# Kernel optimization log

Measured on AMD Instinct MI355X. Metric: run time of the kernel, lower is better.

## Reference

```python
import jax, jax.numpy as jnp
import numpy as np
from jax import lax

B, T = 16, 1000
IN_DIM = 257
CTX = 3            # left + 1 + right
FEAT = CTX * IN_DIM  # 771
H = 512
L = 2              # SRU layers
KN = 9             # conv kernels
KS = 6             # conv kernel size


def setup_inputs() -> dict:
    key = jax.random.key(0)
    ks = jax.random.split(key, 10)
    n = jax.random.normal
    return {
        "inputs": n(ks[0], (B, T, FEAT), jnp.float32),
        "W_in": n(ks[1], (FEAT, H), jnp.float32) / np.sqrt(FEAT),
        "b_in": jnp.zeros((H,), jnp.float32),
        "W_rnn": n(ks[2], (L, H, 3 * H), jnp.float32) / np.sqrt(H),
        "v_rnn": n(ks[3], (L, 2 * H), jnp.float32) * 0.1,
        "b_rnn": jnp.zeros((L, 2 * H), jnp.float32),
        "conv_k": n(ks[4], (KN, 1, KS, KS), jnp.float32) * 0.05,
        "conv_b": jnp.zeros((KN,), jnp.float32),
        "W_out": n(ks[5], (H * KN, FEAT), jnp.float32) / np.sqrt(H * KN),
        "b_out": jnp.zeros((FEAT,), jnp.float32),
    }


def _sru_layer(x, W, v, b):
    # x: (T, B, H) time-major; SRU: c_t = f_t*c_{t-1} + (1-f_t)*(W x_t),
    # highway h_t = r_t*c_t + (1-r_t)*x_t; gates peek at c_{t-1} via v.
    U = jnp.einsum("tbh,hk->tbk", x, W)          # (T, B, 3H)
    xt, fp, rp = jnp.split(U, 3, axis=-1)
    vf, vr = jnp.split(v, 2)
    bf, br = jnp.split(b, 2)

    def step(c, inp):
        xt_t, fp_t, rp_t, xin_t = inp
        f = jax.nn.sigmoid(fp_t + vf * c + bf)
        c_new = f * c + (1.0 - f) * xt_t
        r = jax.nn.sigmoid(rp_t + vr * c + br)
        h = r * c_new + (1.0 - r) * xin_t
        return c_new, h

    c0 = jnp.zeros(x.shape[1:], x.dtype)
    _, hs = lax.scan(step, c0, (xt, fp, rp, x))
    return hs


def reference(inputs, W_in, b_in, W_rnn, v_rnn, b_rnn, conv_k, conv_b, W_out, b_out):
    # input layer: Linear + Tanh
    h = jnp.tanh(jnp.einsum("btf,fh->bth", inputs, W_in) + b_in)  # (B,T,H)
    x = jnp.transpose(h, (1, 0, 2))                               # (T,B,H)
    for l in range(L):
        x = _sru_layer(x, W_rnn[l], v_rnn[l], b_rnn[l])
    h = jnp.transpose(x, (1, 0, 2))[:, None]                      # (B,1,T,H)

    # Conv2d with asymmetric pad (left/top 3, right/bottom 2), +bias, tanh
    y = lax.conv_general_dilated(
        h, conv_k, window_strides=(1, 1), padding=[(3, 2), (3, 2)],
        dimension_numbers=("NCHW", "OIHW", "NCHW"))
    y = jnp.tanh(y + conv_b[None, :, None, None])                 # (B,KN,T,H)
    # MaxPool2d(3, stride=1, padding=1)
    y = lax.reduce_window(y, -jnp.inf, lax.max, (1, 1, 3, 3), (1, 1, 1, 1),
                          [(0, 0), (0, 0), (1, 1), (1, 1)])

    # (B,KN,T,H) -> (B,T,H,KN) -> (B,T,H*KN)  (matches torch double transpose)
    y = jnp.transpose(y, (0, 2, 3, 1)).reshape(B, T, H * KN)
    mask = jax.nn.sigmoid(jnp.einsum("btf,fo->bto", y, W_out) + b_out)
    out = mask * inputs
    return out[:, :, IN_DIM:2 * IN_DIM]  # center frame (left_context slice)
```

## Files before the change

kernel.cpp:

```cpp
#include <hip/hip_runtime.h>
#include <hip/hip_bf16.h>

#define B_    16
#define T_    1000
#define FEAT  771
#define FEATP 800
#define H_    512
#define H3    1536
#define KN_   9
#define KHID  4608
#define M_    16000
#define NOUT  257
#define KSLICES 3

typedef _Float16 half8 __attribute__((ext_vector_type(8)));
typedef _Float16 half4 __attribute__((ext_vector_type(4)));
typedef _Float16 half2v __attribute__((ext_vector_type(2)));
typedef _Float16 h2 __attribute__((ext_vector_type(2)));
typedef float    floatx4 __attribute__((ext_vector_type(4)));

__device__ inline float tanh_fast(float z) {
    return 1.0f - 2.0f / (1.0f + __expf(2.0f * z));
}
__device__ inline float sigmoid_fast(float z) {
    return 1.0f / (1.0f + __expf(-z));
}

__device__ inline void gload16(const _Float16* g, _Float16* l) {
    __builtin_amdgcn_global_load_lds(
        (const __attribute__((address_space(1))) void*)g,
        (__attribute__((address_space(3))) void*)l, 16, 0, 0);
}

__device__ inline void pk_fma_acc(unsigned& acc, unsigned w, unsigned x) {
    asm("v_pk_fma_f16 %0, %1, %2, %0" : "+v"(acc) : "s"(w), "v"(x));
}
__device__ inline unsigned pk_max(unsigned a, unsigned b) {
    unsigned d;
    asm("v_pk_max_f16 %0, %1, %2" : "=v"(d) : "v"(a), "v"(b));
    return d;
}

__global__ void convert_inputs(const float* __restrict__ in, _Float16* __restrict__ A1) {
    size_t i = (size_t)blockIdx.x * 256 + threadIdx.x;
    if (i >= (size_t)M_ * FEATP) return;
    size_t r = i / FEATP;
    int   cc = (int)(i % FEATP);
    A1[i] = (cc < FEAT) ? (_Float16)in[r * FEAT + cc] : (_Float16)0.f;
}

__global__ void pack_ck(const float* __restrict__ ck, unsigned int* __restrict__ ckp) {
    const int i = threadIdx.x;
    if (i < 9 * 36) {
        const _Float16 w = (_Float16)ck[i];
        const unsigned short u = __builtin_bit_cast(unsigned short, w);
        ckp[i] = ((unsigned int)u << 16) | u;
    }
}

__global__ __launch_bounds__(256) void transpose_w(
    const float* __restrict__ W, _Float16* __restrict__ Wt,
    int K, int N, int ldw, int coloff, int Kp, int perm9)
{
    __shared__ float tile[32][33];
    const int kb = blockIdx.x * 32;
    const int nb = blockIdx.y * 32;
    const int tx = threadIdx.x & 31;
    const int ty = threadIdx.x >> 5;
    #pragma unroll
    for (int r = ty; r < 32; r += 8) {
        const int k = kb + r, n = nb + tx;
        tile[r][tx] = (k < K && n < N) ? W[(size_t)k * ldw + coloff + n] : 0.f;
    }
    __syncthreads();
    #pragma unroll
    for (int r = ty; r < 32; r += 8) {
        const int n = nb + r, k = kb + tx;
        if (n < N && k < Kp) {
            size_t kidx = (size_t)k;
            if (perm9) kidx = (size_t)(k % 9) * 512 + (size_t)(k / 9);
            Wt[(size_t)n * Kp + kidx] = (_Float16)tile[tx][r];
        }
    }
}

template <int EPI>
__global__ __launch_bounds__(256) void gemm_kernel(
    const _Float16* __restrict__ A, const _Float16* __restrict__ Bt,
    int Kp, int nk, int Nb,
    _Float16* __restrict__ Ch, float* __restrict__ Cf, int ldc,
    const float* __restrict__ bias)
{
    __shared__ __align__(16) _Float16 As[2][128][32];
    __shared__ __align__(16) _Float16 Bs[2][128][32];

    const int tid  = threadIdx.x;
    const int m0   = blockIdx.x * 128;
    const int n0   = blockIdx.y * 128;
    const int koff = blockIdx.z * (nk << 5);
    const int wave = tid >> 6;
    const int lane = tid & 63;
    const int wr   = (wave >> 1) << 6;
    const int wc   = (wave & 1) << 6;
    const int lrow = lane & 15;
    const int lq   = lane >> 4;

    const int srow0  = wave * 32 + (lane >> 2);
    const int schunk = (lane & 3) * 8;
    const _Float16* aSrc = A  + (size_t)(m0 + srow0) * Kp + koff + schunk;
    const _Float16* bSrc = Bt + (size_t)(n0 + srow0) * Kp + koff + schunk;
    const size_t rstep = (size_t)16 * Kp;

    floatx4 acc[4][4];
    #pragma unroll
    for (int i = 0; i < 4; ++i)
        #pragma unroll
        for (int j = 0; j < 4; ++j)
            #pragma unroll
            for (int r = 0; r < 4; ++r) acc[i][j][r] = 0.f;

    gload16(aSrc,         &As[0][wave * 32][0]);
    gload16(aSrc + rstep, &As[0][wave * 32 + 16][0]);
    gload16(bSrc,         &Bs[0][wave * 32][0]);
    gload16(bSrc + rstep, &Bs[0][wave * 32 + 16][0]);
    asm volatile("s_waitcnt vmcnt(0)" ::: "memory");
    __builtin_amdgcn_s_barrier();

    for (int kc = 0; kc < nk; ++kc) {
        const int cur = kc & 1;
        if (kc + 1 < nk) {
            const _Float16* a2 = aSrc + (size_t)(kc + 1) * 32;
            const _Float16* b2 = bSrc + (size_t)(kc + 1) * 32;
            gload16(a2,         &As[cur ^ 1][wave * 32][0]);
            gload16(a2 + rstep, &As[cur ^ 1][wave * 32 + 16][0]);
            gload16(b2,         &Bs[cur ^ 1][wave * 32][0]);
            gload16(b2 + rstep, &Bs[cur ^ 1][wave * 32 + 16][0]);
        }

        half8 af[4], bfr[4];
        #pragma unroll
        for (int i = 0; i < 4; ++i) af[i]  = *(const half8*)(&As[cur][wr + i * 16 + lrow][lq * 8]);
        #pragma unroll
        for (int j = 0; j < 4; ++j) bfr[j] = *(const half8*)(&Bs[cur][wc + j * 16 + lrow][lq * 8]);
        #pragma unroll
        for (int i = 0; i < 4; ++i)
            #pragma unroll
            for (int j = 0; j < 4; ++j)
                acc[i][j] = __builtin_amdgcn_mfma_f32_16x16x32_f16(af[i], bfr[j], acc[i][j], 0, 0, 0);

        if (kc + 1 < nk) {
            asm volatile("s_waitcnt vmcnt(0)" ::: "memory");
            __builtin_amdgcn_s_barrier();
        }
    }

    #pragma unroll
    for (int j = 0; j < 4; ++j) {
        const int col = n0 + wc + j * 16 + lrow;
        if (col >= Nb) continue;
        #pragma unroll
        for (int i = 0; i < 4; ++i) {
            #pragma unroll
            for (int r = 0; r < 4; ++r) {
                const int row = m0 + wr + i * 16 + lq * 4 + r;
                float v = acc[i][j][r];
                if constexpr (EPI == 0) {
                    float z = v + bias[col];
                    Ch[(size_t)row * ldc + col] = (_Float16)tanh_fast(z);
                } else if constexpr (EPI == 1) {
                    Ch[(size_t)(col >> 9) * ((size_t)M_ * 512) + (size_t)row * 512 + (col & 511)] = (_Float16)v;
                } else {
                    Cf[(size_t)blockIdx.z * M_ * NOUT + (size_t)row * NOUT + col] = v;
                }
            }
        }
    }
}

__global__ __launch_bounds__(256) void reduce_out(
    const float* __restrict__ Cp, const float* __restrict__ bias,
    const float* __restrict__ aux, float* __restrict__ out)
{
    const size_t i = (size_t)blockIdx.x * 256 + threadIdx.x;
    if (i >= (size_t)M_ * NOUT) return;
    const int row = (int)(i / NOUT);
    const int col = (int)(i % NOUT);
    float s = Cp[i] + Cp[i + (size_t)M_ * NOUT] + Cp[i + 2 * (size_t)M_ * NOUT];
    out[i] = sigmoid_fast(s + bias[col]) * aux[(size_t)row * FEAT + 257 + col];
}

__global__ __launch_bounds__(64) void sru_scan(
    const _Float16* __restrict__ U,
    const _Float16* __restrict__ X,
    _Float16* __restrict__ Xout,
    const float* __restrict__ v, const float* __restrict__ bg)
{
    __shared__ __align__(16) _Float16 lds[2][4][40][64];
    const int tid = threadIdx.x;
    const int b   = blockIdx.x >> 3;
    const int h0  = (blockIdx.x & 7) << 6;
    const int h   = h0 + tid;
    const float vf = v[h],       vr = v[512 + h];
    const float bf = bg[h],      br = bg[512 + h];

    const _Float16* plane0 = U;
    const _Float16* plane1 = U + (size_t)M_ * 512;
    const _Float16* plane2 = U + 2 * (size_t)M_ * 512;
    const _Float16* plane3 = X;

    const int lrow = tid >> 3;
    const int lcol = (tid & 7) * 8;

    _Float16* ox = Xout + (size_t)b * T_ * 512 + h;

    auto refill = [&](int bufi, int t0) {
        const size_t rbase = (size_t)(b * T_ + t0 + lrow) * 512 + h0 + lcol;
        #pragma unroll
        for (int j = 0; j < 5; ++j) {
            const size_t o = rbase + (size_t)(8 * j) * 512;
            gload16(plane0 + o, &lds[bufi][0][8 * j][0]);
            gload16(plane1 + o, &lds[bufi][1][8 * j][0]);
            gload16(plane2 + o, &lds[bufi][2][8 * j][0]);
            gload16(plane3 + o, &lds[bufi][3][8 * j][0]);
        }
    };

    refill(0, 0);
    float c = 0.f;
    int cur = 0;
    for (int tb = 0; tb < 25; ++tb) {
        const int t0 = tb * 40;
        if (tb + 1 < 25) {
            refill(cur ^ 1, t0 + 40);
            asm volatile("s_waitcnt vmcnt(20)" ::: "memory");
        } else {
            asm volatile("s_waitcnt vmcnt(0)" ::: "memory");
        }
        __builtin_amdgcn_sched_barrier(0);
        #pragma unroll
        for (int j = 0; j < 40; ++j) {
            const float xt = (float)lds[cur][0][j][tid];
            const float fp = (float)lds[cur][1][j][tid];
            const float rp = (float)lds[cur][2][j][tid];
            const float x  = (float)lds[cur][3][j][tid];
            const float f  = sigmoid_fast(fp + vf * c + bf);
            const float r  = sigmoid_fast(rp + vr * c + br);
            const float cn = f * c + (1.0f - f) * xt;
            const float hO = r * cn + (1.0f - r) * x;
            ox[(size_t)(t0 + j) * 512] = (_Float16)hO;
            c = cn;
        }
        cur ^= 1;
    }
}

#define CVW 76

__global__ __launch_bounds__(320) void conv_pool(
    const _Float16* __restrict__ X, const unsigned int* __restrict__ ckp,
    const float* __restrict__ cb, _Float16* __restrict__ A3)
{
    __shared__ __align__(16) _Float16 in_s[23][80];
    __shared__ __align__(16) _Float16 cv[9][18][CVW];
    const int tid = threadIdx.x;
    int bi = blockIdx.x;
    const int th = bi & 7;  bi >>= 3;
    const int tt = bi % 63;
    const int b  = bi / 63;
    const int t0 = tt * 16, h0 = th * 64;

    for (int i = tid; i < 23 * 76; i += 320) {
        const int r = i / 76, cc = i % 76;
        const int gt = t0 - 4 + r, gh = h0 - 4 + cc;
        _Float16 val = (_Float16)0.f;
        if (gt >= 0 && gt < T_ && gh >= 0 && gh < H_)
            val = X[((size_t)b * T_ + gt) * H_ + gh];
        in_s[r][cc] = val;
    }
    __syncthreads();

    if (tid < 306) {
        const int pt = tid / 17;
        const int co = (tid % 17) * 4;

        const int ct = t0 - 1 + pt;
        const bool rok = (ct >= 0) && (ct < T_);
        const int chb = h0 - 1 + co;
        const bool ok0 = rok && (chb + 0 >= 0) && (chb + 0 < H_);
        const bool ok1 = rok && (chb + 1 >= 0) && (chb + 1 < H_);
        const bool ok2 = rok && (chb + 2 >= 0) && (chb + 2 < H_);
        const bool ok3 = rok && (chb + 3 >= 0) && (chb + 3 < H_);

        unsigned acc0[9], acc1[9];
        #pragma unroll
        for (int k = 0; k < 9; ++k) { acc0[k] = 0u; acc1[k] = 0u; }

        #pragma unroll 1
        for (int ii = 0; ii < 6; ++ii) {
            const unsigned int* rw = (const unsigned int*)&in_s[pt + ii][co];
            const uint2 a01 = *(const uint2*)(rw);
            const uint2 a23 = *(const uint2*)(rw + 2);
            const unsigned int A0 = a01.x, A1v = a01.y, A2 = a23.x, A3v = a23.y;
            const unsigned int A4 = rw[4];
            const unsigned int M0 = __builtin_amdgcn_alignbit(A1v, A0, 16);
            const unsigned int M1 = __builtin_amdgcn_alignbit(A2, A1v, 16);
            const unsigned int M2 = __builtin_amdgcn_alignbit(A3v, A2, 16);
            const unsigned int M3 = __builtin_amdgcn_alignbit(A4, A3v, 16);

            const unsigned int* wt = ckp + ii * 6;
            #pragma unroll
            for (int k = 0; k < 9; ++k) {
                const unsigned int* wk = wt + k * 36;
                pk_fma_acc(acc0[k], wk[0], A0);   pk_fma_acc(acc1[k], wk[0], A1v);
                pk_fma_acc(acc0[k], wk[1], M0);   pk_fma_acc(acc1[k], wk[1], M1);
                pk_fma_acc(acc0[k], wk[2], A1v);  pk_fma_acc(acc1[k], wk[2], A2);
                pk_fma_acc(acc0[k], wk[3], M1);   pk_fma_acc(acc1[k], wk[3], M2);
                pk_fma_acc(acc0[k], wk[4], A2);   pk_fma_acc(acc1[k], wk[4], A3v);
                pk_fma_acc(acc0[k], wk[5], M2);   pk_fma_acc(acc1[k], wk[5], M3);
            }
        }

        const _Float16 NEG = (_Float16)(-65504.f);
        #pragma unroll
        for (int k = 0; k < 9; ++k) {
            const h2 pa = __builtin_bit_cast(h2, acc0[k]);
            const h2 pb = __builtin_bit_cast(h2, acc1[k]);
            half4 o;
            o[0] = ok0 ? pa[0] : NEG;
            o[1] = ok1 ? pa[1] : NEG;
            o[2] = ok2 ? pb[0] : NEG;
            o[3] = ok3 ? pb[1] : NEG;
            *(half4*)(&cv[k][pt][co]) = o;
        }
    }
    __syncthreads();

    if (tid < 256) {
        const int pt = tid >> 4;
        const int gt = t0 + pt;
        if (gt < T_) {
            const int ph = (tid & 15) * 4;
            _Float16* dst = A3 + ((size_t)b * T_ + gt) * KHID + (h0 + ph);
            #pragma unroll
            for (int k = 0; k < 9; ++k) {
                unsigned q01 = 0xFC00FC00u, q23 = 0xFC00FC00u;
                #pragma unroll
                for (int dr = 0; dr < 3; ++dr) {
                    const unsigned* cr = (const unsigned*)&cv[k][pt + dr][ph];
                    const uint2 w01 = *(const uint2*)(cr);
                    const unsigned w2 = cr[2];
                    const unsigned m12 = __builtin_amdgcn_alignbit(w01.y, w01.x, 16);
                    const unsigned m34 = __builtin_amdgcn_alignbit(w2, w01.y, 16);
                    q01 = pk_max(q01, pk_max(pk_max(w01.x, m12), w01.y));
                    q23 = pk_max(q23, pk_max(pk_max(w01.y, m34), w2));
                }
                const h2 qa = __builtin_bit_cast(h2, q01);
                const h2 qb = __builtin_bit_cast(h2, q23);
                const float bk = cb[k];
                half4 o;
                o[0] = (_Float16)tanh_fast((float)qa[0] + bk);
                o[1] = (_Float16)tanh_fast((float)qa[1] + bk);
                o[2] = (_Float16)tanh_fast((float)qb[0] + bk);
                o[3] = (_Float16)tanh_fast((float)qb[1] + bk);
                *(half4*)(dst + (size_t)k * 512) = o;
            }
        }
    }
}

extern "C" void kernel_launch(void* const* d_in, const int* in_sizes, int n_in,
                              void* d_out, int out_size, void* d_ws, size_t ws_size,
                              hipStream_t stream) {
    const float* inputs = (const float*)d_in[0];
    const float* W_in   = (const float*)d_in[1];
    const float* b_in   = (const float*)d_in[2];
    const float* W_rnn  = (const float*)d_in[3];
    const float* v_rnn  = (const float*)d_in[4];
    const float* b_rnn  = (const float*)d_in[5];
    const float* conv_k = (const float*)d_in[6];
    const float* conv_b = (const float*)d_in[7];
    const float* W_out  = (const float*)d_in[8];
    const float* b_out  = (const float*)d_in[9];
    float* out = (float*)d_out;

    char* ws = (char*)d_ws;
    size_t off = 0;
    auto take = [&](size_t bytes) -> char* {
        off = (off + 255) & ~(size_t)255;
        char* p = ws + off;
        off += bytes;
        return p;
    };
    _Float16* W3T  = (_Float16*)take((size_t)NOUT * KHID * 2);
    _Float16* A1   = (_Float16*)take((size_t)M_ * FEATP * 2);
    _Float16* W1T  = (_Float16*)take((size_t)H_ * FEATP * 2);
    _Float16* W2T0 = (_Float16*)take((size_t)H3 * H_ * 2);
    _Float16* W2T1 = (_Float16*)take((size_t)H3 * H_ * 2);
    _Float16* X0   = (_Float16*)take((size_t)M_ * H_ * 2);
    _Float16* X1   = (_Float16*)take((size_t)M_ * H_ * 2);
    _Float16* U    = (_Float16*)take(3 * (size_t)M_ * 512 * 2);
    _Float16* A3   = (_Float16*)take((size_t)M_ * KHID * 2);
    unsigned int* ckp = (unsigned int*)take(9 * 36 * 4);
    float* Cp = (float*)A1;
    _Float16* X2 = X0;

    {
        size_t n = (size_t)M_ * FEATP;
        convert_inputs<<<dim3((unsigned)((n + 255) / 256)), 256, 0, stream>>>(inputs, A1);
    }
    pack_ck<<<dim3(1), 384, 0, stream>>>(conv_k, ckp);
    transpose_w<<<dim3(25, 16), 256, 0, stream>>>(W_in, W1T, FEAT, H_, H_, 0, FEATP, 0);
    transpose_w<<<dim3(16, 48), 256, 0, stream>>>(W_rnn, W2T0, H_, H3, H3, 0, H_, 0);
    transpose_w<<<dim3(16, 48), 256, 0, stream>>>(W_rnn + (size_t)H_ * H3, W2T1, H_, H3, H3, 0, H_, 0);
    transpose_w<<<dim3(144, 9), 256, 0, stream>>>(W_out, W3T, KHID, NOUT, FEAT, 257, KHID, 1);

    gemm_kernel<0><<<dim3(125, 4), 256, 0, stream>>>(A1, W1T, FEATP, 25, H_, X0, nullptr, H_, b_in);

    gemm_kernel<1><<<dim3(125, 12), 256, 0, stream>>>(X0, W2T0, H_, 16, H3, U, nullptr, 0, nullptr);
    sru_scan<<<dim3(128), 64, 0, stream>>>(U, X0, X1, v_rnn, b_rnn);

    gemm_kernel<1><<<dim3(125, 12), 256, 0, stream>>>(X1, W2T1, H_, 16, H3, U, nullptr, 0, nullptr);
    sru_scan<<<dim3(128), 64, 0, stream>>>(U, X1, X2, v_rnn + 1024, b_rnn + 1024);

    conv_pool<<<dim3(16 * 63 * 8), 320, 0, stream>>>(X2, ckp, conv_b, A3);

    gemm_kernel<3><<<dim3(125, 3, KSLICES), 256, 0, stream>>>(A3, W3T, KHID, 144 / KSLICES, NOUT, nullptr, Cp, 0, nullptr);
    {
        const unsigned nred = (unsigned)(((size_t)M_ * NOUT + 255) / 256);
        reduce_out<<<dim3(nred), 256, 0, stream>>>(Cp, b_out + 257, inputs, out);
    }
}
```

Baseline: 727.0 us.

## Skip dead MFMA tiles in ragged output GEMM, fuse setup kernels, cut split-K

The final GEMM gains a ragged mode in which waves and 16-column fragments lying entirely past N=257 skip their LDS loads and MFMAs, removing wasted tensor work in the third N-block. Split-K drops from 3 to 2 slices, so the reduce pass reads one fewer partial buffer at the cost of fewer blocks in flight. The conv-kernel packing is folded into the input-convert kernel, and the two RNN weight transposes are merged into one launch, reducing launch count. The maxpool is reordered to take the vertical max first and then the horizontal one, sharing work across the two output pairs.

```diff
diff --git a/kernel.cpp b/kernel.cpp
--- a/kernel.cpp
+++ b/kernel.cpp
@@ -11,7 +11,7 @@
 #define KHID  4608
 #define M_    16000
 #define NOUT  257
-#define KSLICES 3
+#define KSLICES 2
 
 typedef _Float16 half8 __attribute__((ext_vector_type(8)));
 typedef _Float16 half4 __attribute__((ext_vector_type(4)));
@@ -41,7 +41,15 @@
     return d;
 }
 
-__global__ void convert_inputs(const float* __restrict__ in, _Float16* __restrict__ A1) {
+__global__ void convert_inputs(const float* __restrict__ in, _Float16* __restrict__ A1,
+                               const float* __restrict__ ck, unsigned int* __restrict__ ckp) {
+    if (blockIdx.x == 0) {
+        for (int j = threadIdx.x; j < 9 * 36; j += 256) {
+            const _Float16 w = (_Float16)ck[j];
+            const unsigned short u = __builtin_bit_cast(unsigned short, w);
+            ckp[j] = ((unsigned int)u << 16) | u;
+        }
+    }
     size_t i = (size_t)blockIdx.x * 256 + threadIdx.x;
     if (i >= (size_t)M_ * FEATP) return;
     size_t r = i / FEATP;
@@ -49,19 +57,13 @@
     A1[i] = (cc < FEAT) ? (_Float16)in[r * FEAT + cc] : (_Float16)0.f;
 }
 
-__global__ void pack_ck(const float* __restrict__ ck, unsigned int* __restrict__ ckp) {
-    const int i = threadIdx.x;
-    if (i < 9 * 36) {
-        const _Float16 w = (_Float16)ck[i];
-        const unsigned short u = __builtin_bit_cast(unsigned short, w);
-        ckp[i] = ((unsigned int)u << 16) | u;
-    }
-}
-
 __global__ __launch_bounds__(256) void transpose_w(
     const float* __restrict__ W, _Float16* __restrict__ Wt,
-    int K, int N, int ldw, int coloff, int Kp, int perm9)
+    int K, int N, int ldw, int coloff, int Kp, int perm9,
+    size_t zsrc, size_t zdst)
 {
+    W  += (size_t)blockIdx.z * zsrc;
+    Wt += (size_t)blockIdx.z * zdst;
     __shared__ float tile[32][33];
     const int kb = blockIdx.x * 32;
     const int nb = blockIdx.y * 32;
@@ -84,7 +86,7 @@
     }
 }
 
-template <int EPI>
+template <int EPI, int RAG>
 __global__ __launch_bounds__(256) void gemm_kernel(
     const _Float16* __restrict__ A, const _Float16* __restrict__ Bt,
     int Kp, int nk, int Nb,
@@ -104,6 +106,7 @@
     const int wc   = (wave & 1) << 6;
     const int lrow = lane & 15;
     const int lq   = lane >> 4;
+    const bool waveAlive = !RAG || (n0 + wc < Nb);
 
     const int srow0  = wave * 32 + (lane >> 2);
     const int schunk = (lane & 3) * 8;
@@ -137,16 +140,23 @@
             gload16(b2 + rstep, &Bs[cur ^ 1][wave * 32 + 16][0]);
         }
 
-        half8 af[4], bfr[4];
-        #pragma unroll
-        for (int i = 0; i < 4; ++i) af[i]  = *(const half8*)(&As[cur][wr + i * 16 + lrow][lq * 8]);
-        #pragma unroll
-        for (int j = 0; j < 4; ++j) bfr[j] = *(const half8*)(&Bs[cur][wc + j * 16 + lrow][lq * 8]);
-        #pragma unroll
-        for (int i = 0; i < 4; ++i)
-            #pragma unroll
-            for (int j = 0; j < 4; ++j)
-                acc[i][j] = __builtin_amdgcn_mfma_f32_16x16x32_f16(af[i], bfr[j], acc[i][j], 0, 0, 0);
+        if (waveAlive) {
+            half8 af[4], bfr[4];
+            #pragma unroll
+            for (int i = 0; i < 4; ++i) af[i] = *(const half8*)(&As[cur][wr + i * 16 + lrow][lq * 8]);
+            #pragma unroll
+            for (int j = 0; j < 4; ++j) {
+                if (RAG && n0 + wc + j * 16 >= Nb) continue;
+                bfr[j] = *(const half8*)(&Bs[cur][wc + j * 16 + lrow][lq * 8]);
+            }
+            #pragma unroll
+            for (int i = 0; i < 4; ++i)
+                #pragma unroll
+                for (int j = 0; j < 4; ++j) {
+                    if (RAG && n0 + wc + j * 16 >= Nb) continue;
+                    acc[i][j] = __builtin_amdgcn_mfma_f32_16x16x32_f16(af[i], bfr[j], acc[i][j], 0, 0, 0);
+                }
+        }
 
         if (kc + 1 < nk) {
             asm volatile("s_waitcnt vmcnt(0)" ::: "memory");
@@ -185,7 +195,7 @@
     if (i >= (size_t)M_ * NOUT) return;
     const int row = (int)(i / NOUT);
     const int col = (int)(i % NOUT);
-    float s = Cp[i] + Cp[i + (size_t)M_ * NOUT] + Cp[i + 2 * (size_t)M_ * NOUT];
+    float s = Cp[i] + Cp[i + (size_t)M_ * NOUT];
     out[i] = sigmoid_fast(s + bias[col]) * aux[(size_t)row * FEAT + 257 + col];
 }
 
@@ -343,17 +353,19 @@
             _Float16* dst = A3 + ((size_t)b * T_ + gt) * KHID + (h0 + ph);
             #pragma unroll
             for (int k = 0; k < 9; ++k) {
-                unsigned q01 = 0xFC00FC00u, q23 = 0xFC00FC00u;
-                #pragma unroll
-                for (int dr = 0; dr < 3; ++dr) {
-                    const unsigned* cr = (const unsigned*)&cv[k][pt + dr][ph];
-                    const uint2 w01 = *(const uint2*)(cr);
-                    const unsigned w2 = cr[2];
-                    const unsigned m12 = __builtin_amdgcn_alignbit(w01.y, w01.x, 16);
-                    const unsigned m34 = __builtin_amdgcn_alignbit(w2, w01.y, 16);
-                    q01 = pk_max(q01, pk_max(pk_max(w01.x, m12), w01.y));
-                    q23 = pk_max(q23, pk_max(pk_max(w01.y, m34), w2));
-                }
+                const unsigned* c0 = (const unsigned*)&cv[k][pt + 0][ph];
+                const unsigned* c1 = (const unsigned*)&cv[k][pt + 1][ph];
+                const unsigned* c2 = (const unsigned*)&cv[k][pt + 2][ph];
+                const uint2 x0 = *(const uint2*)c0;  const unsigned y0 = c0[2];
+                const uint2 x1 = *(const uint2*)c1;  const unsigned y1 = c1[2];
+                const uint2 x2 = *(const uint2*)c2;  const unsigned y2 = c2[2];
+                const unsigned VA = pk_max(pk_max(x0.x, x1.x), x2.x);
+                const unsigned VB = pk_max(pk_max(x0.y, x1.y), x2.y);
+                const unsigned VC = pk_max(pk_max(y0,   y1),   y2);
+                const unsigned m12 = __builtin_amdgcn_alignbit(VB, VA, 16);
+                const unsigned m34 = __builtin_amdgcn_alignbit(VC, VB, 16);
+                const unsigned q01 = pk_max(pk_max(VA, m12), VB);
+                const unsigned q23 = pk_max(pk_max(VB, m34), VC);
                 const h2 qa = __builtin_bit_cast(h2, q01);
                 const h2 qb = __builtin_bit_cast(h2, q23);
                 const float bk = cb[k];
@@ -406,25 +418,24 @@
 
     {
         size_t n = (size_t)M_ * FEATP;
-        convert_inputs<<<dim3((unsigned)((n + 255) / 256)), 256, 0, stream>>>(inputs, A1);
-    }
-    pack_ck<<<dim3(1), 384, 0, stream>>>(conv_k, ckp);
-    transpose_w<<<dim3(25, 16), 256, 0, stream>>>(W_in, W1T, FEAT, H_, H_, 0, FEATP, 0);
-    transpose_w<<<dim3(16, 48), 256, 0, stream>>>(W_rnn, W2T0, H_, H3, H3, 0, H_, 0);
-    transpose_w<<<dim3(16, 48), 256, 0, stream>>>(W_rnn + (size_t)H_ * H3, W2T1, H_, H3, H3, 0, H_, 0);
-    transpose_w<<<dim3(144, 9), 256, 0, stream>>>(W_out, W3T, KHID, NOUT, FEAT, 257, KHID, 1);
-
-    gemm_kernel<0><<<dim3(125, 4), 256, 0, stream>>>(A1, W1T, FEATP, 25, H_, X0, nullptr, H_, b_in);
-
-    gemm_kernel<1><<<dim3(125, 12), 256, 0, stream>>>(X0, W2T0, H_, 16, H3, U, nullptr, 0, nullptr);
+        convert_inputs<<<dim3((unsigned)((n + 255) / 256)), 256, 0, stream>>>(inputs, A1, conv_k, ckp);
+    }
+    transpose_w<<<dim3(25, 16), 256, 0, stream>>>(W_in, W1T, FEAT, H_, H_, 0, FEATP, 0, 0, 0);
+    transpose_w<<<dim3(16, 48, 2), 256, 0, stream>>>(W_rnn, W2T0, H_, H3, H3, 0, H_, 0,
+                                                     (size_t)H_ * H3, (size_t)H3 * H_);
+    transpose_w<<<dim3(144, 9), 256, 0, stream>>>(W_out, W3T, KHID, NOUT, FEAT, 257, KHID, 1, 0, 0);
+
+    gemm_kernel<0, 0><<<dim3(125, 4), 256, 0, stream>>>(A1, W1T, FEATP, 25, H_, X0, nullptr, H_, b_in);
+
+    gemm_kernel<1, 0><<<dim3(125, 12), 256, 0, stream>>>(X0, W2T0, H_, 16, H3, U, nullptr, 0, nullptr);
     sru_scan<<<dim3(128), 64, 0, stream>>>(U, X0, X1, v_rnn, b_rnn);
 
-    gemm_kernel<1><<<dim3(125, 12), 256, 0, stream>>>(X1, W2T1, H_, 16, H3, U, nullptr, 0, nullptr);
+    gemm_kernel<1, 0><<<dim3(125, 12), 256, 0, stream>>>(X1, W2T1, H_, 16, H3, U, nullptr, 0, nullptr);
     sru_scan<<<dim3(128), 64, 0, stream>>>(U, X1, X2, v_rnn + 1024, b_rnn + 1024);
 
     conv_pool<<<dim3(16 * 63 * 8), 320, 0, stream>>>(X2, ckp, conv_b, A3);
 
-    gemm_kernel<3><<<dim3(125, 3, KSLICES), 256, 0, stream>>>(A3, W3T, KHID, 144 / KSLICES, NOUT, nullptr, Cp, 0, nullptr);
+    gemm_kernel<3, 1><<<dim3(125, 3, KSLICES), 256, 0, stream>>>(A3, W3T, KHID, 144 / KSLICES, NOUT, nullptr, Cp, 0, nullptr);
     {
         const unsigned nred = (unsigned)(((size_t)M_ * NOUT + 255) / 256);
         reduce_out<<<dim3(nred), 256, 0, stream>>>(Cp, b_out + 257, inputs, out);
```

New measurement: 690.2 us (median of 3 runs). 1.05x faster.
